# Performance work log

Measured on AMD Instinct MI355X. Metric: run time of the kernel, lower is better.

The kernel has to match this reference:

```python
import jax, jax.numpy as jnp
import numpy as np

N_NODES = 100000
N_EDGES = 625000
IN_CH = 128
OUT_CH = 128


def setup_inputs() -> dict:
    key = jax.random.key(0)
    k1, k2, k3, k4, k5 = jax.random.split(key, 5)
    node_embeddings = jax.random.normal(k1, (N_NODES, IN_CH), dtype=jnp.float32)
    edge_index = jax.random.randint(k2, (2, N_EDGES), 0, N_NODES, dtype=jnp.int64)
    attn_weights = jax.random.normal(k3, (IN_CH,), dtype=jnp.float32)
    # torch Linear default init: U(-1/sqrt(fan_in), 1/sqrt(fan_in))
    bound = 1.0 / np.sqrt(IN_CH)
    W = jax.random.uniform(k4, (OUT_CH, IN_CH), dtype=jnp.float32, minval=-bound, maxval=bound)
    b = jax.random.uniform(k5, (OUT_CH,), dtype=jnp.float32, minval=-bound, maxval=bound)
    return {"node_embeddings": node_embeddings, "edge_index": edge_index,
            "attn_weights": attn_weights, "W": W, "b": b}


def reference(node_embeddings, edge_index, attn_weights, W, b):
    # softmax over the per-feature attention weights (dim=-1)
    a = jax.nn.softmax(attn_weights)                      # [d]
    src = node_embeddings[edge_index[0]]                  # [E, d] gather
    tgt = node_embeddings[edge_index[1]]                  # [E, d] gather
    edge_attr = (src + tgt) * a                           # fused weighted sum
    out = jnp.einsum('ed,od->eo', edge_attr, W) + b       # Linear
    return jax.nn.relu(out)
```

## Files before the change

kernel.cpp:

```cpp
#include <hip/hip_runtime.h>
#include <hip/hip_fp16.h>
#include <cstdint>

#define NCH 128
#define NSLICE 8

typedef short short8v __attribute__((ext_vector_type(8)));
typedef unsigned short ushort4v __attribute__((ext_vector_type(4)));
typedef float f32x4  __attribute__((ext_vector_type(4)));

static __device__ __forceinline__ short f2bf(float f) {
    unsigned u = __float_as_uint(f);
    u += 0x7FFFu + ((u >> 16) & 1u);
    return (short)(u >> 16);
}
static __device__ __forceinline__ unsigned short f2h(float f) {
    return __half_as_ushort(__float2half(f));
}
static __device__ __forceinline__ float h2f(unsigned short u) {
    return __half2float(__ushort_as_half(u));
}

static __device__ __forceinline__ ushort4v gather8_l2(const unsigned short* p) {
    unsigned long long v = __hip_atomic_load(
        reinterpret_cast<const unsigned long long*>(p),
        __ATOMIC_RELAXED, __HIP_MEMORY_SCOPE_AGENT);
    return __builtin_bit_cast(ushort4v, v);
}

__global__ __launch_bounds__(128)
void prep_kernel(const float* __restrict__ aw,
                 const float* __restrict__ W,
                 short* __restrict__ Wpb) {
    __shared__ float sa[NCH];
    const int t = threadIdx.x;
    const int o = blockIdx.x;
    sa[t] = aw[t];
    __syncthreads();
    float m = -1e30f;
#pragma unroll
    for (int d = 0; d < NCH; ++d) m = fmaxf(m, sa[d]);
    float s = 0.f;
#pragma unroll
    for (int d = 0; d < NCH; ++d) s += expf(sa[d] - m);
    const float av = expf(sa[t] - m) / s;
    Wpb[o * NCH + t] = f2bf(W[o * NCH + t] * av);
}

__global__ __launch_bounds__(256)
void node_gemm_mfma(const float* __restrict__ X,
                    const short* __restrict__ Wpb,
                    const float* __restrict__ bias,
                    unsigned short* __restrict__ Ys, int M) {
    const int t    = threadIdx.x;
    const int wave = t >> 6;
    const int lane = t & 63;
    const int r    = lane & 15;
    const int kb   = lane >> 4;

    const int node  = blockIdx.x * 64 + wave * 16 + r;
    const int nodec = node < M ? node : M - 1;
    const float* xr = X + (size_t)nodec * NCH;

    short8v b[4];
#pragma unroll
    for (int ks = 0; ks < 4; ++ks) {
        const float4 f0 = *reinterpret_cast<const float4*>(xr + ks * 32 + kb * 8);
        const float4 f1 = *reinterpret_cast<const float4*>(xr + ks * 32 + kb * 8 + 4);
        short8v v;
        v[0] = f2bf(f0.x); v[1] = f2bf(f0.y); v[2] = f2bf(f0.z); v[3] = f2bf(f0.w);
        v[4] = f2bf(f1.x); v[5] = f2bf(f1.y); v[6] = f2bf(f1.z); v[7] = f2bf(f1.w);
        b[ks] = v;
    }

#pragma unroll
    for (int tile = 0; tile < 8; ++tile) {
        f32x4 acc = {0.f, 0.f, 0.f, 0.f};
        const short* wr = Wpb + (size_t)(tile * 16 + r) * NCH;
#pragma unroll
        for (int ks = 0; ks < 4; ++ks) {
            const short8v a = *reinterpret_cast<const short8v*>(wr + ks * 32 + kb * 8);
            acc = __builtin_amdgcn_mfma_f32_16x16x32_bf16(a, b[ks], acc, 0, 0, 0);
        }
        if (node < M) {
            const float4 vb = *reinterpret_cast<const float4*>(bias + tile * 16 + kb * 4);
            ushort4v h;
            h[0] = f2h(acc[0] + 0.5f * vb.x);
            h[1] = f2h(acc[1] + 0.5f * vb.y);
            h[2] = f2h(acc[2] + 0.5f * vb.z);
            h[3] = f2h(acc[3] + 0.5f * vb.w);
            *reinterpret_cast<ushort4v*>(
                Ys + (size_t)tile * M * 16 + (size_t)node * 16 + kb * 4) = h;
        }
    }
}

__global__ __launch_bounds__(256)
void edge_out_sliced(const unsigned short* __restrict__ Ys,
                     const int* __restrict__ ei,
                     float* __restrict__ out, int E, int M) {
    const unsigned bid = blockIdx.x;
    const int slice = bid & (NSLICE - 1);
    const int eblk  = bid >> 3;
    const int t  = threadIdx.x;
    const int cl = t & 3;
    const int e0 = eblk * 256 + (t >> 2);

    const unsigned short* base = Ys + (size_t)slice * M * 16 + cl * 4;

    int s[4], g[4];
#pragma unroll
    for (int k = 0; k < 4; ++k) {
        const int e = e0 + k * 64;
        const int ec = e < E ? e : 0;
        s[k] = ei[ec];
        g[k] = ei[E + ec];
    }
    ushort4v hs[4], ht[4];
#pragma unroll
    for (int k = 0; k < 4; ++k) {
        hs[k] = gather8_l2(base + (size_t)s[k] * 16);
        ht[k] = gather8_l2(base + (size_t)g[k] * 16);
    }
#pragma unroll
    for (int k = 0; k < 4; ++k) {
        const int e = e0 + k * 64;
        if (e < E) {
            f32x4 r;
            r[0] = fmaxf(h2f(hs[k][0]) + h2f(ht[k][0]), 0.f);
            r[1] = fmaxf(h2f(hs[k][1]) + h2f(ht[k][1]), 0.f);
            r[2] = fmaxf(h2f(hs[k][2]) + h2f(ht[k][2]), 0.f);
            r[3] = fmaxf(h2f(hs[k][3]) + h2f(ht[k][3]), 0.f);
            f32x4* dst = reinterpret_cast<f32x4*>(
                out + (size_t)e * NCH + slice * 16 + cl * 4);
            __builtin_nontemporal_store(r, dst);
        }
    }
}

__global__ __launch_bounds__(256)
void direct_edge_kernel(const float* __restrict__ X,
                        const int* __restrict__ ei,
                        const float* __restrict__ aw,
                        const float* __restrict__ W,
                        const float* __restrict__ bias,
                        float* __restrict__ out, int E) {
    __shared__ float sW[NCH][NCH + 1];
    __shared__ float sa[NCH];
    __shared__ float sE[8][NCH + 4];
    const int t = threadIdx.x;
    if (t < NCH) sa[t] = aw[t];
    __syncthreads();
    float m = -1e30f;
#pragma unroll
    for (int d = 0; d < NCH; ++d) m = fmaxf(m, sa[d]);
    float ssum = 0.f;
#pragma unroll
    for (int d = 0; d < NCH; ++d) ssum += expf(sa[d] - m);
    const float av = (t < NCH) ? expf(sa[t] - m) / ssum : 0.f;
    __syncthreads();
    if (t < NCH) sa[t] = av;
    __syncthreads();
    for (int i = t; i < NCH * 32; i += 256) {
        const int o = i >> 5, q = i & 31;
        float4 v = reinterpret_cast<const float4*>(W)[o * 32 + q];
        sW[o][q * 4 + 0] = v.x * sa[q * 4 + 0];
        sW[o][q * 4 + 1] = v.y * sa[q * 4 + 1];
        sW[o][q * 4 + 2] = v.z * sa[q * 4 + 2];
        sW[o][q * 4 + 3] = v.w * sa[q * 4 + 3];
    }
    __syncthreads();
    const int le = t >> 5, q = t & 31;
    for (int e0 = blockIdx.x * 8; e0 < E; e0 += gridDim.x * 8) {
        const int e = e0 + le;
        if (e < E) {
            const int s = ei[e];
            const int g = ei[E + e];
            const float4 vs = reinterpret_cast<const float4*>(X)[(size_t)s * 32 + q];
            const float4 vt = reinterpret_cast<const float4*>(X)[(size_t)g * 32 + q];
            sE[le][q * 4 + 0] = vs.x + vt.x;
            sE[le][q * 4 + 1] = vs.y + vt.y;
            sE[le][q * 4 + 2] = vs.z + vt.z;
            sE[le][q * 4 + 3] = vs.w + vt.w;
        }
        __syncthreads();
        if (e < E) {
            float a0 = 0.f, a1 = 0.f, a2 = 0.f, a3 = 0.f;
            const int o = q * 4;
#pragma unroll 4
            for (int d = 0; d < NCH; ++d) {
                const float x = sE[le][d];
                a0 += x * sW[o + 0][d];
                a1 += x * sW[o + 1][d];
                a2 += x * sW[o + 2][d];
                a3 += x * sW[o + 3][d];
            }
            float4 r;
            r.x = fmaxf(a0 + bias[o + 0], 0.f);
            r.y = fmaxf(a1 + bias[o + 1], 0.f);
            r.z = fmaxf(a2 + bias[o + 2], 0.f);
            r.w = fmaxf(a3 + bias[o + 3], 0.f);
            reinterpret_cast<float4*>(out)[(size_t)e * 32 + q] = r;
        }
        __syncthreads();
    }
}

extern "C" void kernel_launch(void* const* d_in, const int* in_sizes, int n_in,
                              void* d_out, int out_size, void* d_ws, size_t ws_size,
                              hipStream_t stream) {
    const float* X    = (const float*)d_in[0];
    const int*   ei   = (const int*)d_in[1];
    const float* aw   = (const float*)d_in[2];
    const float* W    = (const float*)d_in[3];
    const float* bias = (const float*)d_in[4];
    float* out = (float*)d_out;

    const int M = in_sizes[0] / NCH;
    const int E = in_sizes[1] / 2;

    const size_t y_off   = 65536;
    const size_t y_bytes = (size_t)M * NCH * sizeof(unsigned short);

    if (ws_size >= y_off + y_bytes) {
        short* Wpb = (short*)d_ws;
        unsigned short* Ys = (unsigned short*)((char*)d_ws + y_off);
        prep_kernel<<<NCH, 128, 0, stream>>>(aw, W, Wpb);
        node_gemm_mfma<<<(M + 63) / 64, 256, 0, stream>>>(X, Wpb, bias, Ys, M);
        const int eblks = (E + 255) / 256;
        edge_out_sliced<<<eblks * NSLICE, 256, 0, stream>>>(Ys, ei, out, E, M);
    } else {
        int grid = (E + 7) / 8;
        if (grid > 32768) grid = 32768;
        direct_edge_kernel<<<grid, 256, 0, stream>>>(X, ei, aw, W, bias, out, E);
    }
}
```

Before: 126.0 us.

## Stage weights in swizzled LDS and process two node groups per wave

The node GEMM kernel now copies the 128x128 bf16 weight matrix into shared memory with an XOR swizzle, instead of reading it from global memory per lane. Each wave computes two 16-node groups that share each weight fragment, so a block covers 128 nodes and the grid is halved. This cuts global and L2 weight traffic and reuses A operands across two MFMAs. The cost is a 32KB LDS fill per block, which can limit occupancy.

```diff
diff --git a/kernel.cpp b/kernel.cpp
--- a/kernel.cpp
+++ b/kernel.cpp
@@ -52,45 +52,75 @@
                     const short* __restrict__ Wpb,
                     const float* __restrict__ bias,
                     unsigned short* __restrict__ Ys, int M) {
-    const int t    = threadIdx.x;
+    __shared__ short sW[NCH * NCH];
+    const int t = threadIdx.x;
+
+    for (int it = 0; it < 8; ++it) {
+        const int j   = it * 256 + t;
+        const int row = j >> 4;
+        const int cc  = j & 15;
+        const int scc = cc ^ (row & 7);
+        *reinterpret_cast<short8v*>(&sW[row * NCH + scc * 8]) =
+            *reinterpret_cast<const short8v*>(Wpb + (size_t)j * 8);
+    }
+    __syncthreads();
+
     const int wave = t >> 6;
     const int lane = t & 63;
     const int r    = lane & 15;
     const int kb   = lane >> 4;
 
-    const int node  = blockIdx.x * 64 + wave * 16 + r;
-    const int nodec = node < M ? node : M - 1;
-    const float* xr = X + (size_t)nodec * NCH;
-
-    short8v b[4];
-#pragma unroll
-    for (int ks = 0; ks < 4; ++ks) {
-        const float4 f0 = *reinterpret_cast<const float4*>(xr + ks * 32 + kb * 8);
-        const float4 f1 = *reinterpret_cast<const float4*>(xr + ks * 32 + kb * 8 + 4);
-        short8v v;
-        v[0] = f2bf(f0.x); v[1] = f2bf(f0.y); v[2] = f2bf(f0.z); v[3] = f2bf(f0.w);
-        v[4] = f2bf(f1.x); v[5] = f2bf(f1.y); v[6] = f2bf(f1.z); v[7] = f2bf(f1.w);
-        b[ks] = v;
+    const int nbase = blockIdx.x * 128 + wave * 32;
+
+    short8v b[2][4];
+    int node[2];
+#pragma unroll
+    for (int ng = 0; ng < 2; ++ng) {
+        node[ng] = nbase + ng * 16 + r;
+        const int nodec = node[ng] < M ? node[ng] : M - 1;
+        const float* xr = X + (size_t)nodec * NCH;
+#pragma unroll
+        for (int ks = 0; ks < 4; ++ks) {
+            const float4 f0 = *reinterpret_cast<const float4*>(xr + ks * 32 + kb * 8);
+            const float4 f1 = *reinterpret_cast<const float4*>(xr + ks * 32 + kb * 8 + 4);
+            short8v v;
+            v[0] = f2bf(f0.x); v[1] = f2bf(f0.y); v[2] = f2bf(f0.z); v[3] = f2bf(f0.w);
+            v[4] = f2bf(f1.x); v[5] = f2bf(f1.y); v[6] = f2bf(f1.z); v[7] = f2bf(f1.w);
+            b[ng][ks] = v;
+        }
     }
 
 #pragma unroll
     for (int tile = 0; tile < 8; ++tile) {
-        f32x4 acc = {0.f, 0.f, 0.f, 0.f};
-        const short* wr = Wpb + (size_t)(tile * 16 + r) * NCH;
+        f32x4 acc0 = {0.f, 0.f, 0.f, 0.f};
+        f32x4 acc1 = {0.f, 0.f, 0.f, 0.f};
+        const int row = tile * 16 + r;
 #pragma unroll
         for (int ks = 0; ks < 4; ++ks) {
-            const short8v a = *reinterpret_cast<const short8v*>(wr + ks * 32 + kb * 8);
-            acc = __builtin_amdgcn_mfma_f32_16x16x32_bf16(a, b[ks], acc, 0, 0, 0);
-        }
-        if (node < M) {
-            const float4 vb = *reinterpret_cast<const float4*>(bias + tile * 16 + kb * 4);
+            const int cc = ks * 4 + kb;
+            const short8v a = *reinterpret_cast<const short8v*>(
+                &sW[row * NCH + (cc ^ (row & 7)) * 8]);
+            acc0 = __builtin_amdgcn_mfma_f32_16x16x32_bf16(a, b[0][ks], acc0, 0, 0, 0);
+            acc1 = __builtin_amdgcn_mfma_f32_16x16x32_bf16(a, b[1][ks], acc1, 0, 0, 0);
+        }
+        const float4 vb = *reinterpret_cast<const float4*>(bias + tile * 16 + kb * 4);
+        if (node[0] < M) {
             ushort4v h;
-            h[0] = f2h(acc[0] + 0.5f * vb.x);
-            h[1] = f2h(acc[1] + 0.5f * vb.y);
-            h[2] = f2h(acc[2] + 0.5f * vb.z);
-            h[3] = f2h(acc[3] + 0.5f * vb.w);
+            h[0] = f2h(acc0[0] + 0.5f * vb.x);
+            h[1] = f2h(acc0[1] + 0.5f * vb.y);
+            h[2] = f2h(acc0[2] + 0.5f * vb.z);
+            h[3] = f2h(acc0[3] + 0.5f * vb.w);
             *reinterpret_cast<ushort4v*>(
-                Ys + (size_t)tile * M * 16 + (size_t)node * 16 + kb * 4) = h;
+                Ys + (size_t)tile * M * 16 + (size_t)node[0] * 16 + kb * 4) = h;
+        }
+        if (node[1] < M) {
+            ushort4v h;
+            h[0] = f2h(acc1[0] + 0.5f * vb.x);
+            h[1] = f2h(acc1[1] + 0.5f * vb.y);
+            h[2] = f2h(acc1[2] + 0.5f * vb.z);
+            h[3] = f2h(acc1[3] + 0.5f * vb.w);
+            *reinterpret_cast<ushort4v*>(
+                Ys + (size_t)tile * M * 16 + (size_t)node[1] * 16 + kb * 4) = h;
         }
     }
 }
@@ -226,7 +256,7 @@
         short* Wpb = (short*)d_ws;
         unsigned short* Ys = (unsigned short*)((char*)d_ws + y_off);
         prep_kernel<<<NCH, 128, 0, stream>>>(aw, W, Wpb);
-        node_gemm_mfma<<<(M + 63) / 64, 256, 0, stream>>>(X, Wpb, bias, Ys, M);
+        node_gemm_mfma<<<(M + 127) / 128, 256, 0, stream>>>(X, Wpb, bias, Ys, M);
         const int eblks = (E + 255) / 256;
         edge_out_sliced<<<eblks * NSLICE, 256, 0, stream>>>(Ys, ei, out, E, M);
     } else {
```

Result: faster. 106.8 us (-15.3%).
